# Kernel tuning notes

Measured on AMD Instinct MI355X. Metric: run time of the kernel, lower is better.

Reference implementation:

```python
import math
import jax, jax.numpy as jnp
import numpy as np

B, L, D, H = 2, 2048, 1024, 16
HD = D // H  # 64

def setup_inputs() -> dict:
    key = jax.random.key(0)
    k1, k2, k3 = jax.random.split(key, 3)
    x = jax.random.normal(k1, (B, L, D), dtype=jnp.float32)
    Wqkv = jax.random.normal(k2, (3 * D, D), dtype=jnp.float32) * (1.0 / math.sqrt(D))
    Wo = jax.random.normal(k3, (D, D), dtype=jnp.float32) * (1.0 / math.sqrt(D))
    return {"x": x, "Wqkv": Wqkv, "Wo": Wo}

def reference(x, Wqkv, Wo):
    # QKV projection (torch Linear: y = x @ W.T), then split
    qkv = jnp.einsum('bld,ed->ble', x, Wqkv)  # [B, L, 3D]
    q, k, v = jnp.split(qkv, 3, axis=-1)
    # [B, H, L, HD]
    q = q.reshape(B, L, H, HD).transpose(0, 2, 1, 3)
    k = k.reshape(B, L, H, HD).transpose(0, 2, 1, 3)
    v = v.reshape(B, L, H, HD).transpose(0, 2, 1, 3)
    # scores; causal mask applied before the 1/sqrt(d) scale (as in source;
    # -inf is unchanged by scaling so math matches scale-then-mask)
    scores = jnp.einsum('bhqd,bhkd->bhqk', q, k)
    causal = jnp.tril(jnp.ones((L, L), dtype=bool))
    scores = jnp.where(causal, scores, -jnp.inf)
    attn = jax.nn.softmax(scores / math.sqrt(HD), axis=-1)
    out = jnp.einsum('bhqk,bhkd->bhqd', attn, v)  # [B, H, L, HD]
    out = out.transpose(0, 2, 1, 3).reshape(B, L, D)
    # output projection (dropout is identity in eval / p=0)
    return jnp.einsum('bld,ed->ble', out, Wo)
```

## Files before the change

### kernel.cpp

```cpp
#include <hip/hip_runtime.h>
#include <hip/hip_bf16.h>
#include <cstdint>
#include <cstddef>

#define B_SZ 2
#define L_SEQ 2048
#define DM 1024
#define NH 16
#define HDIM 64
#define BL (B_SZ * L_SEQ)
#define QKV_N (3 * DM)

typedef __attribute__((ext_vector_type(4))) float f32x4;
typedef __attribute__((ext_vector_type(16))) float f32x16;
typedef __attribute__((ext_vector_type(8))) short bf16x8;
typedef __attribute__((ext_vector_type(4))) unsigned int u32x4;
typedef unsigned short u16;
typedef __attribute__((ext_vector_type(4))) unsigned short u16x4;

__device__ __forceinline__ float bf2f(u16 u) {
  union { unsigned int i; float f; } c; c.i = ((unsigned int)u) << 16; return c.f;
}
__device__ __forceinline__ u16 f2bf(float f) {
  union { float f; unsigned int i; } c; c.f = f;
  unsigned int r = c.i + 0x7fffu + ((c.i >> 16) & 1u);
  return (u16)(r >> 16);
}

__device__ __forceinline__ void gload_lds16(const void* g, void* l) {
  __builtin_amdgcn_global_load_lds(
      (const __attribute__((address_space(1))) void*)g,
      (__attribute__((address_space(3))) void*)l, 16, 0, 0);
}

__device__ __forceinline__ f32x16 mfma32(bf16x8 a, bf16x8 b, f32x16 c) {
  return __builtin_amdgcn_mfma_f32_32x32x16_bf16(a, b, c, 0, 0, 0);
}

__device__ __forceinline__ unsigned cvtpk(float lo, float hi) {
  unsigned r;
  asm("v_cvt_pk_bf16_f32 %0, %1, %2" : "=v"(r) : "v"(lo), "v"(hi));
  return r;
}
__device__ __forceinline__ void plswap(unsigned& a, unsigned& b) {
  asm("v_permlane32_swap_b32 %0, %1" : "+v"(a), "+v"(b));
}

template <int BASE>
__device__ __forceinline__ bf16x8 pack_bfrag(const f32x16& v) {
  unsigned a  = cvtpk(v[BASE + 0], v[BASE + 1]);
  unsigned a2 = cvtpk(v[BASE + 2], v[BASE + 3]);
  unsigned b  = cvtpk(v[BASE + 4], v[BASE + 5]);
  unsigned b2 = cvtpk(v[BASE + 6], v[BASE + 7]);
  plswap(a, b);
  plswap(a2, b2);
  u32x4 fw; fw[0] = a; fw[1] = a2; fw[2] = b; fw[3] = b2;
  return __builtin_bit_cast(bf16x8, fw);
}

__global__ __launch_bounds__(256) void cvt_f32_bf16(const float* __restrict__ in,
                                                    u16* __restrict__ out, int n4) {
  int i = blockIdx.x * blockDim.x + threadIdx.x;
  const int stride = gridDim.x * blockDim.x;
  for (; i < n4; i += stride) {
    float4 v = ((const float4*)in)[i];
    u16x4 o;
    o[0] = f2bf(v.x); o[1] = f2bf(v.y); o[2] = f2bf(v.z); o[3] = f2bf(v.w);
    ((u16x4*)out)[i] = o;
  }
}

template <bool BF16_OUT>
__global__ __launch_bounds__(256) void gemm_bt(
    const u16* __restrict__ A, const u16* __restrict__ B,
    void* __restrict__ Cv, int M, int N, int K) {
  __shared__ u16 As[128 * 32];
  __shared__ u16 Bs[128 * 32];
  const int tid = threadIdx.x;
  const int lane = tid & 63, w = tid >> 6;
  const int lr = lane & 15, lg = lane >> 4;
  const int wr = w >> 1, wc = w & 1;
  const int bm = blockIdx.y * 128, bn = blockIdx.x * 128;

  f32x4 acc[4][4] = {};

  const int l4 = lane >> 2;
  const int csw = ((lane & 3) ^ ((lane >> 3) & 3)) * 8;
  const size_t aoff0 = (size_t)(bm + (w * 2 + 0) * 16 + l4) * K + csw;
  const size_t aoff1 = (size_t)(bm + (w * 2 + 1) * 16 + l4) * K + csw;
  const size_t boff0 = (size_t)(bn + (w * 2 + 0) * 16 + l4) * K + csw;
  const size_t boff1 = (size_t)(bn + (w * 2 + 1) * 16 + l4) * K + csw;
  u16* As0 = As + (w * 2 + 0) * 512;
  u16* As1 = As + (w * 2 + 1) * 512;
  u16* Bs0 = Bs + (w * 2 + 0) * 512;
  u16* Bs1 = Bs + (w * 2 + 1) * 512;
  const int sw_rd = (lr >> 1) & 3;

  for (int k0 = 0; k0 < K; k0 += 32) {
    gload_lds16(A + aoff0 + k0, As0);
    gload_lds16(A + aoff1 + k0, As1);
    gload_lds16(B + boff0 + k0, Bs0);
    gload_lds16(B + boff1 + k0, Bs1);
    __syncthreads();

    bf16x8 af[4], bfr[4];
#pragma unroll
    for (int mt = 0; mt < 4; ++mt) {
      const int row = wr * 64 + mt * 16 + lr;
      af[mt] = *(const bf16x8*)&As[row * 32 + ((lg ^ sw_rd) * 8)];
    }
#pragma unroll
    for (int nt = 0; nt < 4; ++nt) {
      const int row = wc * 64 + nt * 16 + lr;
      bfr[nt] = *(const bf16x8*)&Bs[row * 32 + ((lg ^ sw_rd) * 8)];
    }
#pragma unroll
    for (int mt = 0; mt < 4; ++mt)
#pragma unroll
      for (int nt = 0; nt < 4; ++nt)
        acc[mt][nt] = __builtin_amdgcn_mfma_f32_16x16x32_bf16(af[mt], bfr[nt],
                                                              acc[mt][nt], 0, 0, 0);
    __syncthreads();
  }

#pragma unroll
  for (int mt = 0; mt < 4; ++mt)
#pragma unroll
    for (int nt = 0; nt < 4; ++nt)
#pragma unroll
      for (int r = 0; r < 4; ++r) {
        const int row = bm + wr * 64 + mt * 16 + lg * 4 + r;
        const int col = bn + wc * 64 + nt * 16 + lr;
        if (BF16_OUT)
          ((u16*)Cv)[(size_t)row * N + col] = f2bf(acc[mt][nt][r]);
        else
          ((float*)Cv)[(size_t)row * N + col] = acc[mt][nt][r];
      }
}

__global__ __launch_bounds__(256) void attn_fused(const u16* __restrict__ qkv,
                                                  u16* __restrict__ aout) {
  __shared__ u16 Kl[2][64 * 64];
  __shared__ u16 Vt[2][64 * 64];

  const int tid = threadIdx.x;
  const int lane = tid & 63, w = tid >> 6;
  const int l31 = lane & 31, hi = lane >> 5;
  const int id = (int)blockIdx.x;
  const int bh = id & 31, slot = id >> 5;
  const int qt = slot < 8 ? 15 - 2 * slot : 2 * (slot - 8);
  const int b = bh >> 4, h = bh & 15;
  const u16* base = qkv + (size_t)b * L_SEQ * QKV_N;
  const int W = qt * 128 + w * 32;
  const int nt = 2 * qt + 2;
  const int qrow = W + l31;

  const u16* kf_src = base + (size_t)(w * 16 + (lane >> 3)) * QKV_N + DM +
                      h * HDIM + (((lane & 7) ^ (lane >> 3)) * 8);
  auto stage_K = [&](int t, int buf) {
    const u16* s = kf_src + (size_t)t * 64 * QKV_N;
    gload_lds16(s, &Kl[buf][w * 1024]);
    gload_lds16(s + (size_t)8 * QKV_N, &Kl[buf][w * 1024 + 512]);
  };

  const int vd0 = (tid & 31) * 2;
  const int vkb = tid >> 5;
  const int vge = tid & 7;
  const int vgo = (tid & 7) ^ 4;
  const u16* gpv_base = base + (size_t)(vkb * 8) * QKV_N + 2 * DM + h * HDIM + vd0;
  unsigned int vtmp[8];

  auto issue_V = [&](int t) {
    const u16* gpv = gpv_base + (size_t)t * 64 * QKV_N;
#pragma unroll
    for (int j = 0; j < 8; ++j)
      vtmp[j] = *(const unsigned int*)(gpv + (size_t)j * QKV_N);
  };
  auto write_V = [&](int buf) {
    u32x4 lo, hiw;
#pragma unroll
    for (int j = 0; j < 4; ++j) {
      lo[j]  = __builtin_amdgcn_perm(vtmp[2 * j + 1], vtmp[2 * j], 0x05040100u);
      hiw[j] = __builtin_amdgcn_perm(vtmp[2 * j + 1], vtmp[2 * j], 0x07060302u);
    }
    *(u32x4*)&Vt[buf][vd0 * 64 + ((vkb ^ vge) * 8)] = lo;
    *(u32x4*)&Vt[buf][(vd0 + 1) * 64 + ((vkb ^ vgo) * 8)] = hiw;
  };

  bf16x8 bq[4];
  {
    const u16* qp = base + (size_t)qrow * QKV_N + h * HDIM + hi * 8;
#pragma unroll
    for (int dc = 0; dc < 4; ++dc) {
      bf16x8 tq = *(const bf16x8*)(qp + dc * 16);
#pragma unroll
      for (int i = 0; i < 8; ++i)
        tq[i] = (short)f2bf(bf2f((u16)tq[i]) * 0.18033688f);
      bq[dc] = tq;
    }
  }

  f32x16 acc0 = {}, acc1 = {};
  float mrow = -1e30f, lrow = 0.f;

  const int vg = ((l31 >> 1) & 7) ^ ((l31 & 1) << 2);
  const int lsw = l31 & 7;

  stage_K(0, 0);
  issue_V(0);
  write_V(0);
  __syncthreads();

  for (int t = 0; t < nt; ++t) {
    const int cur = t & 1;
    if (t + 1 < nt) {
      stage_K(t + 1, cur ^ 1);
      issue_V(t + 1);
    }

    if (64 * t <= W + 31) {
      f32x16 s0 = {}, s1 = {};
      __builtin_amdgcn_s_setprio(1);
#pragma unroll
      for (int dc = 0; dc < 4; ++dc) {
        const int sl = ((dc * 2 + hi) ^ lsw) * 8;
        const bf16x8 k0 = *(const bf16x8*)&Kl[cur][l31 * 64 + sl];
        const bf16x8 k1 = *(const bf16x8*)&Kl[cur][(32 + l31) * 64 + sl];
        s0 = mfma32(k0, bq[dc], s0);
        s1 = mfma32(k1, bq[dc], s1);
      }
      __builtin_amdgcn_s_setprio(0);

      if (64 * t + 63 > W) {
#pragma unroll
        for (int r = 0; r < 16; ++r) {
          const int kg = t * 64 + (r & 3) + 8 * (r >> 2) + 4 * hi;
          if (kg > qrow) s0[r] = -1e30f;
          if (kg + 32 > qrow) s1[r] = -1e30f;
        }
      }

      float mx[8];
#pragma unroll
      for (int i = 0; i < 8; ++i)
        mx[i] = fmaxf(fmaxf(s0[i], s0[i + 8]), fmaxf(s1[i], s1[i + 8]));
#pragma unroll
      for (int i = 0; i < 4; ++i) mx[i] = fmaxf(mx[i], mx[i + 4]);
      float px = fmaxf(fmaxf(mx[0], mx[2]), fmaxf(mx[1], mx[3]));
      px = fmaxf(px, __shfl_xor(px, 32));

      if (!__all(px <= mrow + 8.f)) {
        const float mnew = fmaxf(mrow, px);
        const float alpha = exp2f(mrow - mnew);
        mrow = mnew;
        lrow *= alpha;
#pragma unroll
        for (int i = 0; i < 16; ++i) { acc0[i] *= alpha; acc1[i] *= alpha; }
      }

#pragma unroll
      for (int r = 0; r < 16; ++r) {
        s0[r] = exp2f(s0[r] - mrow);
        s1[r] = exp2f(s1[r] - mrow);
      }
      float sm[8];
#pragma unroll
      for (int i = 0; i < 8; ++i)
        sm[i] = (s0[i] + s0[i + 8]) + (s1[i] + s1[i + 8]);
#pragma unroll
      for (int i = 0; i < 4; ++i) sm[i] += sm[i + 4];
      float rs = (sm[0] + sm[2]) + (sm[1] + sm[3]);
      rs += __shfl_xor(rs, 32);
      lrow += rs;

      const bf16x8 pf0 = pack_bfrag<0>(s0);
      const bf16x8 pf1 = pack_bfrag<8>(s0);
      const bf16x8 pf2 = pack_bfrag<0>(s1);
      const bf16x8 pf3 = pack_bfrag<8>(s1);

      __builtin_amdgcn_s_setprio(1);
#pragma unroll
      for (int c = 0; c < 4; ++c) {
        const bf16x8 pf = c == 0 ? pf0 : c == 1 ? pf1 : c == 2 ? pf2 : pf3;
        const int sl = ((c * 2 + hi) ^ vg) * 8;
        const bf16x8 va = *(const bf16x8*)&Vt[cur][l31 * 64 + sl];
        const bf16x8 vb = *(const bf16x8*)&Vt[cur][(32 + l31) * 64 + sl];
        acc0 = mfma32(va, pf, acc0);
        acc1 = mfma32(vb, pf, acc1);
      }
      __builtin_amdgcn_s_setprio(0);
    }

    if (t + 1 < nt) write_V(cur ^ 1);
    __syncthreads();
  }

  const float inv = 1.f / lrow;
#pragma unroll
  for (int i = 0; i < 16; ++i) { acc0[i] *= inv; acc1[i] *= inv; }
  const bf16x8 of0 = pack_bfrag<0>(acc0);
  const bf16x8 of1 = pack_bfrag<8>(acc0);
  const bf16x8 of2 = pack_bfrag<0>(acc1);
  const bf16x8 of3 = pack_bfrag<8>(acc1);
  u16* op = aout + (size_t)(b * L_SEQ + qrow) * DM + h * HDIM + hi * 8;
  *(bf16x8*)(op + 0)  = of0;
  *(bf16x8*)(op + 16) = of1;
  *(bf16x8*)(op + 32) = of2;
  *(bf16x8*)(op + 48) = of3;
}

extern "C" void kernel_launch(void* const* d_in, const int* in_sizes, int n_in,
                              void* d_out, int out_size, void* d_ws, size_t ws_size,
                              hipStream_t stream) {
  (void)in_sizes; (void)n_in; (void)out_size; (void)ws_size;
  const float* x = (const float*)d_in[0];
  const float* wqkv = (const float*)d_in[1];
  const float* wo = (const float*)d_in[2];

  char* ws = (char*)d_ws;
  u16* x_bf = (u16*)(ws);
  u16* w_bf = (u16*)(ws + (size_t)(8u << 20));
  u16* wo_bf = (u16*)(ws + (size_t)(14u << 20));
  u16* qkv_bf = (u16*)(ws + (size_t)(16u << 20));
  u16* ao_bf = x_bf;

  cvt_f32_bf16<<<2048, 256, 0, stream>>>(x, x_bf, BL * DM / 4);
  cvt_f32_bf16<<<2048, 256, 0, stream>>>(wqkv, w_bf, QKV_N * DM / 4);
  cvt_f32_bf16<<<1024, 256, 0, stream>>>(wo, wo_bf, DM * DM / 4);

  dim3 g1(QKV_N / 128, BL / 128);
  gemm_bt<true><<<g1, 256, 0, stream>>>(x_bf, w_bf, (void*)qkv_bf, BL, QKV_N, DM);

  attn_fused<<<dim3(512), 256, 0, stream>>>(qkv_bf, ao_bf);

  dim3 g3(DM / 128, BL / 128);
  gemm_bt<false><<<g3, 256, 0, stream>>>(ao_bf, wo_bf, d_out, BL, DM, DM);
}
```

Before: 149.9 us.

## Split long causal query tiles across two KV-range blocks with a combine pass

Long query tiles (qt>=8) are now split into two blocks covering disjoint KV ranges, and a lookup table assigns 768 blocks so per-block work is more even. Partial unnormalized outputs and (max, sum) statistics go to scratch (d_out and workspace), and a new combine kernel merges them into the bf16 attention output. K staging also switches from direct global-to-LDS loads to register loads with swizzled LDS stores, and the setprio hints are removed. The aim is to fix tail imbalance across CUs, at the cost of an extra launch and the fp32 partial-output traffic.

```diff
diff --git a/kernel.cpp b/kernel.cpp
--- a/kernel.cpp
+++ b/kernel.cpp
@@ -138,8 +138,17 @@
       }
 }
 
+__device__ const uint8_t JQT[24] = {15,14,13,12,11,10,9,8, 7, 15, 14,6, 13,5,
+                                    12,4, 11,3, 10,2, 9,1, 8,0};
+__device__ const uint8_t JT0[24] = {0,0,0,0,0,0,0,0, 0, 16, 16,0, 16,0,
+                                    16,0, 16,0, 16,0, 16,0, 16,0};
+__device__ const uint8_t JT1[24] = {16,16,16,16,16,16,16,16, 16, 32, 30,14, 28,12,
+                                    26,10, 24,8, 22,6, 20,4, 18,2};
+
 __global__ __launch_bounds__(256) void attn_fused(const u16* __restrict__ qkv,
-                                                  u16* __restrict__ aout) {
+                                                  u16* __restrict__ aout,
+                                                  float* __restrict__ opart,
+                                                  float2* __restrict__ mlb) {
   __shared__ u16 Kl[2][64 * 64];
   __shared__ u16 Vt[2][64 * 64];
 
@@ -147,21 +156,19 @@
   const int lane = tid & 63, w = tid >> 6;
   const int l31 = lane & 31, hi = lane >> 5;
   const int id = (int)blockIdx.x;
-  const int bh = id & 31, slot = id >> 5;
-  const int qt = slot < 8 ? 15 - 2 * slot : 2 * (slot - 8);
+  const int bh = id & 31, j = id >> 5;
+  const int qt = JQT[j];
+  const int t0 = JT0[j], t1 = JT1[j];
   const int b = bh >> 4, h = bh & 15;
   const u16* base = qkv + (size_t)b * L_SEQ * QKV_N;
   const int W = qt * 128 + w * 32;
-  const int nt = 2 * qt + 2;
   const int qrow = W + l31;
 
-  const u16* kf_src = base + (size_t)(w * 16 + (lane >> 3)) * QKV_N + DM +
-                      h * HDIM + (((lane & 7) ^ (lane >> 3)) * 8);
-  auto stage_K = [&](int t, int buf) {
-    const u16* s = kf_src + (size_t)t * 64 * QKV_N;
-    gload_lds16(s, &Kl[buf][w * 1024]);
-    gload_lds16(s + (size_t)8 * QKV_N, &Kl[buf][w * 1024 + 512]);
-  };
+  const int krow = tid >> 2;
+  const int ks0 = (tid & 3) * 2;
+  const int kr7 = krow & 7;
+  const u16* gpk_base = base + (size_t)krow * QKV_N + DM + h * HDIM + ks0 * 8;
+  bf16x8 kr0, kr1;
 
   const int vd0 = (tid & 31) * 2;
   const int vkb = tid >> 5;
@@ -170,18 +177,23 @@
   const u16* gpv_base = base + (size_t)(vkb * 8) * QKV_N + 2 * DM + h * HDIM + vd0;
   unsigned int vtmp[8];
 
-  auto issue_V = [&](int t) {
+  auto issue_loads = [&](int t) {
+    const u16* gpk = gpk_base + (size_t)t * 64 * QKV_N;
+    kr0 = *(const bf16x8*)(gpk);
+    kr1 = *(const bf16x8*)(gpk + 8);
     const u16* gpv = gpv_base + (size_t)t * 64 * QKV_N;
 #pragma unroll
-    for (int j = 0; j < 8; ++j)
-      vtmp[j] = *(const unsigned int*)(gpv + (size_t)j * QKV_N);
+    for (int jj = 0; jj < 8; ++jj)
+      vtmp[jj] = *(const unsigned int*)(gpv + (size_t)jj * QKV_N);
   };
-  auto write_V = [&](int buf) {
+  auto write_lds = [&](int buf) {
+    *(bf16x8*)&Kl[buf][krow * 64 + ((ks0 ^ kr7) * 8)] = kr0;
+    *(bf16x8*)&Kl[buf][krow * 64 + (((ks0 + 1) ^ kr7) * 8)] = kr1;
     u32x4 lo, hiw;
 #pragma unroll
-    for (int j = 0; j < 4; ++j) {
-      lo[j]  = __builtin_amdgcn_perm(vtmp[2 * j + 1], vtmp[2 * j], 0x05040100u);
-      hiw[j] = __builtin_amdgcn_perm(vtmp[2 * j + 1], vtmp[2 * j], 0x07060302u);
+    for (int jj = 0; jj < 4; ++jj) {
+      lo[jj]  = __builtin_amdgcn_perm(vtmp[2 * jj + 1], vtmp[2 * jj], 0x05040100u);
+      hiw[jj] = __builtin_amdgcn_perm(vtmp[2 * jj + 1], vtmp[2 * jj], 0x07060302u);
     }
     *(u32x4*)&Vt[buf][vd0 * 64 + ((vkb ^ vge) * 8)] = lo;
     *(u32x4*)&Vt[buf][(vd0 + 1) * 64 + ((vkb ^ vgo) * 8)] = hiw;
@@ -206,21 +218,16 @@
   const int vg = ((l31 >> 1) & 7) ^ ((l31 & 1) << 2);
   const int lsw = l31 & 7;
 
-  stage_K(0, 0);
-  issue_V(0);
-  write_V(0);
+  issue_loads(t0);
+  write_lds(0);
   __syncthreads();
 
-  for (int t = 0; t < nt; ++t) {
-    const int cur = t & 1;
-    if (t + 1 < nt) {
-      stage_K(t + 1, cur ^ 1);
-      issue_V(t + 1);
-    }
+  for (int t = t0; t < t1; ++t) {
+    const int cur = (t - t0) & 1;
+    if (t + 1 < t1) issue_loads(t + 1);
 
     if (64 * t <= W + 31) {
       f32x16 s0 = {}, s1 = {};
-      __builtin_amdgcn_s_setprio(1);
 #pragma unroll
       for (int dc = 0; dc < 4; ++dc) {
         const int sl = ((dc * 2 + hi) ^ lsw) * 8;
@@ -229,7 +236,6 @@
         s0 = mfma32(k0, bq[dc], s0);
         s1 = mfma32(k1, bq[dc], s1);
       }
-      __builtin_amdgcn_s_setprio(0);
 
       if (64 * t + 63 > W) {
 #pragma unroll
@@ -278,7 +284,6 @@
       const bf16x8 pf2 = pack_bfrag<0>(s1);
       const bf16x8 pf3 = pack_bfrag<8>(s1);
 
-      __builtin_amdgcn_s_setprio(1);
 #pragma unroll
       for (int c = 0; c < 4; ++c) {
         const bf16x8 pf = c == 0 ? pf0 : c == 1 ? pf1 : c == 2 ? pf2 : pf3;
@@ -288,25 +293,70 @@
         acc0 = mfma32(va, pf, acc0);
         acc1 = mfma32(vb, pf, acc1);
       }
-      __builtin_amdgcn_s_setprio(0);
-    }
-
-    if (t + 1 < nt) write_V(cur ^ 1);
+    }
+
+    if (t + 1 < t1) write_lds(((t + 1) - t0) & 1);
     __syncthreads();
   }
 
-  const float inv = 1.f / lrow;
-#pragma unroll
-  for (int i = 0; i < 16; ++i) { acc0[i] *= inv; acc1[i] *= inv; }
-  const bf16x8 of0 = pack_bfrag<0>(acc0);
-  const bf16x8 of1 = pack_bfrag<8>(acc0);
-  const bf16x8 of2 = pack_bfrag<0>(acc1);
-  const bf16x8 of3 = pack_bfrag<8>(acc1);
-  u16* op = aout + (size_t)(b * L_SEQ + qrow) * DM + h * HDIM + hi * 8;
-  *(bf16x8*)(op + 0)  = of0;
-  *(bf16x8*)(op + 16) = of1;
-  *(bf16x8*)(op + 32) = of2;
-  *(bf16x8*)(op + 48) = of3;
+  if (qt >= 8) {
+    const int c = (t0 == 16) ? 1 : 0;
+    const int slot = ((qt - 8) * 2 + c) * 32 + bh;
+    float* po = opart + (size_t)slot * 8192 + (w * 32 + l31);
+#pragma unroll
+    for (int i = 0; i < 16; ++i) {
+      const int d0 = (i & 3) + 8 * (i >> 2) + 4 * hi;
+      po[d0 * 128] = acc0[i];
+      po[(d0 + 32) * 128] = acc1[i];
+    }
+    if (hi == 0) mlb[slot * 128 + w * 32 + l31] = make_float2(mrow, lrow);
+  } else {
+    const float inv = 1.f / lrow;
+#pragma unroll
+    for (int i = 0; i < 16; ++i) { acc0[i] *= inv; acc1[i] *= inv; }
+    const bf16x8 of0 = pack_bfrag<0>(acc0);
+    const bf16x8 of1 = pack_bfrag<8>(acc0);
+    const bf16x8 of2 = pack_bfrag<0>(acc1);
+    const bf16x8 of3 = pack_bfrag<8>(acc1);
+    u16* op = aout + (size_t)(b * L_SEQ + qrow) * DM + h * HDIM + hi * 8;
+    *(bf16x8*)(op + 0)  = of0;
+    *(bf16x8*)(op + 16) = of1;
+    *(bf16x8*)(op + 32) = of2;
+    *(bf16x8*)(op + 48) = of3;
+  }
+}
+
+__global__ __launch_bounds__(256) void attn_combine(
+    const float* __restrict__ opart, const float2* __restrict__ mlb,
+    u16* __restrict__ aout) {
+  const int gw = ((int)blockIdx.x * 256 + (int)threadIdx.x) >> 6;
+  const int lane = threadIdx.x & 63;
+  const int u = gw >> 1, qh = gw & 1;
+  const int qt = 8 + (u >> 5), bh = u & 31;
+  const int b = bh >> 4, h = bh & 15;
+  const int s1 = ((qt - 8) * 2) * 32 + bh, s2 = s1 + 32;
+  const int q = qh * 64 + lane;
+  const float2 ml1 = mlb[s1 * 128 + q];
+  const float2 ml2 = mlb[s2 * 128 + q];
+  const float m = fmaxf(ml1.x, ml2.x);
+  const float a1 = exp2f(ml1.x - m), a2 = exp2f(ml2.x - m);
+  const float invl = 1.f / (ml1.y * a1 + ml2.y * a2);
+  const float c1 = a1 * invl, c2 = a2 * invl;
+  const float* p1 = opart + (size_t)s1 * 8192 + q;
+  const float* p2 = opart + (size_t)s2 * 8192 + q;
+  const int qrow = qt * 128 + q;
+  u16* op = aout + (size_t)(b * L_SEQ + qrow) * DM + h * HDIM;
+#pragma unroll
+  for (int d0 = 0; d0 < 64; d0 += 8) {
+    u16x4 o0, o1;
+#pragma unroll
+    for (int jj = 0; jj < 4; ++jj) {
+      o0[jj] = f2bf(p1[(d0 + jj) * 128] * c1 + p2[(d0 + jj) * 128] * c2);
+      o1[jj] = f2bf(p1[(d0 + 4 + jj) * 128] * c1 + p2[(d0 + 4 + jj) * 128] * c2);
+    }
+    *(u16x4*)(op + d0) = o0;
+    *(u16x4*)(op + d0 + 4) = o1;
+  }
 }
 
 extern "C" void kernel_launch(void* const* d_in, const int* in_sizes, int n_in,
@@ -323,6 +373,8 @@
   u16* wo_bf = (u16*)(ws + (size_t)(14u << 20));
   u16* qkv_bf = (u16*)(ws + (size_t)(16u << 20));
   u16* ao_bf = x_bf;
+  float* opart = (float*)d_out;
+  float2* mlb = (float2*)(ws + (size_t)(8u << 20));
 
   cvt_f32_bf16<<<2048, 256, 0, stream>>>(x, x_bf, BL * DM / 4);
   cvt_f32_bf16<<<2048, 256, 0, stream>>>(wqkv, w_bf, QKV_N * DM / 4);
@@ -331,7 +383,8 @@
   dim3 g1(QKV_N / 128, BL / 128);
   gemm_bt<true><<<g1, 256, 0, stream>>>(x_bf, w_bf, (void*)qkv_bf, BL, QKV_N, DM);
 
-  attn_fused<<<dim3(512), 256, 0, stream>>>(qkv_bf, ao_bf);
+  attn_fused<<<dim3(768), 256, 0, stream>>>(qkv_bf, ao_bf, opart, mlb);
+  attn_combine<<<dim3(128), 256, 0, stream>>>(opart, mlb, ao_bf);
 
   dim3 g3(DM / 128, BL / 128);
   gemm_bt<false><<<g3, 256, 0, stream>>>(ao_bf, wo_bf, d_out, BL, DM, DM);
```

Measured after the change: 138.6 us. -7.5%, faster.
